# Optimization experiments

Hardware: AMD Instinct MI355X
Metric: run time of the kernel (lower is better)

The kernel has to match this reference:

```python
import jax, jax.numpy as jnp
import numpy as np

N, M, D = 131072, 512, 128  # points, codebook size, feature dim


def setup_inputs() -> dict:
    key = jax.random.key(0)
    k1, k2 = jax.random.split(key)
    X = jax.random.normal(k1, (N, D), dtype=jnp.float32)
    samples = jax.random.normal(k2, (M, D), dtype=jnp.float32)
    return {"X": X, "samples": samples}


def reference(X, samples):
    # Pairwise L2 distance: sum((x - s)^2, axis=-1) ** (1/2), vectorized via
    # for p=2, without materializing an [N, M, D] tensor).
    x2 = jnp.sum(X * X, axis=1, keepdims=True)              # [N, 1]
    s2 = jnp.sum(samples * samples, axis=1)[None, :]        # [1, M]
    d2 = x2 + s2 - 2.0 * (X @ samples.T)                    # [N, M]
    m_dis = jnp.sqrt(jnp.maximum(d2, 0.0))                  # [N, M]
    # soft=True branch: softmax over axis=0 (across points), as in the original.
    return jax.nn.softmax(-m_dis, axis=0)
```

## Files before the change

kernel.cpp:

```cpp
#include <hip/hip_runtime.h>
#include <hip/hip_bf16.h>

#define NPTS 131072
#define MCB  512
#define DIM  128
#define NRB  (NPTS/128)
#define NCBK (MCB/128)
#define NBLK (NRB*NCBK)

typedef __attribute__((ext_vector_type(4))) float  f32x4;
typedef __attribute__((ext_vector_type(8))) __bf16 bf16x8;
typedef unsigned short u16;
typedef unsigned int   u32;

__device__ __forceinline__ u32 swz(u32 p) { return p ^ (((p >> 8) & 7u) << 4); }

__global__ __launch_bounds__(256) void convert_rows(const float* __restrict__ in,
                                                    u16* __restrict__ outb,
                                                    float* __restrict__ sq,
                                                    int nrows) {
  int wv = threadIdx.x >> 6, ln = threadIdx.x & 63;
  int half = ln >> 5, li = ln & 31;
  int npairs = nrows >> 1;
  for (int pr = blockIdx.x * 4 + wv; pr < npairs; pr += gridDim.x * 4) {
    int row = pr * 2 + half;
    const float4 v = *(const float4*)(in + (size_t)row * DIM + li * 4);
    __hip_bfloat16 b0 = __float2bfloat16(v.x);
    __hip_bfloat16 b1 = __float2bfloat16(v.y);
    __hip_bfloat16 b2 = __float2bfloat16(v.z);
    __hip_bfloat16 b3 = __float2bfloat16(v.w);
    ushort4 o;
    o.x = *(const u16*)&b0; o.y = *(const u16*)&b1;
    o.z = *(const u16*)&b2; o.w = *(const u16*)&b3;
    *(ushort4*)(outb + (size_t)row * DIM + li * 4) = o;
    float f0 = __bfloat162float(b0), f1 = __bfloat162float(b1);
    float f2 = __bfloat162float(b2), f3 = __bfloat162float(b3);
    float s = f0 * f0 + f1 * f1 + f2 * f2 + f3 * f3;
    s += __shfl_xor(s, 1); s += __shfl_xor(s, 2); s += __shfl_xor(s, 4);
    s += __shfl_xor(s, 8); s += __shfl_xor(s, 16);
    if (li == 0) sq[row] = s;
  }
}

template <int WRITE>
__global__ __launch_bounds__(256, 2) void gemm_pass(const u16* __restrict__ Xb,
                                                    const u16* __restrict__ Sb,
                                                    const float* __restrict__ x2,
                                                    const float* __restrict__ s2,
                                                    const float* __restrict__ invs,
                                                    float* __restrict__ outp) {
  __shared__ u16 At[128 * DIM];
  __shared__ u16 Bt[128 * DIM];
  __shared__ float lx2[128], ls2[128], lscale[128], colsum[128];

  int t = threadIdx.x, wv = t >> 6, ln = t & 63;
  u32 h = blockIdx.x;
  u32 l = (h & 7u) * (NBLK / 8) + (h >> 3);
  u32 rb = l >> 2, cb = l & 3u;
  u32 n0 = rb * 128, m0 = cb * 128;

  const char* Ag = (const char*)(Xb + (size_t)n0 * DIM);
  const char* Bg = (const char*)(Sb + (size_t)m0 * DIM);
#pragma unroll
  for (int i = 0; i < 8; i++) {
    u32 c = i * 4 + wv;
    u32 lb = c * 1024;
    u32 go = swz(lb + ln * 16);
    __builtin_amdgcn_global_load_lds((const __attribute__((address_space(1))) void*)(Ag + go),
                                     (__attribute__((address_space(3))) void*)((char*)At + lb),
                                     16, 0, 0);
    __builtin_amdgcn_global_load_lds((const __attribute__((address_space(1))) void*)(Bg + go),
                                     (__attribute__((address_space(3))) void*)((char*)Bt + lb),
                                     16, 0, 0);
  }
  if (t < 128) {
    lx2[t] = x2[n0 + t];
    ls2[t] = s2[m0 + t];
    if (WRITE) lscale[t] = invs[m0 + t];
    else       colsum[t] = 0.f;
  }
  __syncthreads();

  int wr = wv >> 1, wc = wv & 1;
  int rbw = wr * 64, cbw = wc * 64;
  int lr = ln & 15, lg = ln >> 4;

  f32x4 acc[4][4];
#pragma unroll
  for (int i = 0; i < 4; i++)
#pragma unroll
    for (int j = 0; j < 4; j++) acc[i][j] = (f32x4){0.f, 0.f, 0.f, 0.f};

#pragma unroll
  for (int kk = 0; kk < 4; kk++) {
    bf16x8 af[4], bfr[4];
#pragma unroll
    for (int i = 0; i < 4; i++)
      af[i] = *(const bf16x8*)((const char*)At +
               swz((u32)((rbw + i * 16 + lr) * 256 + kk * 64 + lg * 16)));
#pragma unroll
    for (int j = 0; j < 4; j++)
      bfr[j] = *(const bf16x8*)((const char*)Bt +
               swz((u32)((cbw + j * 16 + lr) * 256 + kk * 64 + lg * 16)));
#pragma unroll
    for (int i = 0; i < 4; i++)
#pragma unroll
      for (int j = 0; j < 4; j++)
        acc[i][j] = __builtin_amdgcn_mfma_f32_16x16x32_bf16(af[i], bfr[j], acc[i][j], 0, 0, 0);
  }

  float csum[4] = {0.f, 0.f, 0.f, 0.f};
#pragma unroll
  for (int i = 0; i < 4; i++) {
#pragma unroll
    for (int j = 0; j < 4; j++) {
#pragma unroll
      for (int r = 0; r < 4; r++) {
        int nl = rbw + i * 16 + lg * 4 + r;
        int ml = cbw + j * 16 + lr;
        float d2 = lx2[nl] + ls2[ml] - 2.f * acc[i][j][r];
        d2 = fmaxf(d2, 0.f);
        float e = __expf(-__fsqrt_rn(d2));
        if (WRITE) {
          outp[(size_t)(n0 + nl) * MCB + (m0 + ml)] = e * lscale[ml];
        } else {
          csum[j] += e;
        }
      }
    }
  }
  if (!WRITE) {
#pragma unroll
    for (int j = 0; j < 4; j++) {
      float v = csum[j];
      v += __shfl_xor(v, 16);
      v += __shfl_xor(v, 32);
      if (ln < 16) atomicAdd(&colsum[cbw + j * 16 + ln], v);
    }
    __syncthreads();
    if (t < 128) outp[(size_t)rb * MCB + m0 + t] = colsum[t];
  }
}

__global__ __launch_bounds__(256) void reduce_cols(const float* __restrict__ partial,
                                                   float* __restrict__ invs) {
  int m = blockIdx.x, t = threadIdx.x;
  float s = 0.f;
  for (int k = t; k < NRB; k += 256) s += partial[(size_t)k * MCB + m];
  s += __shfl_xor(s, 1);  s += __shfl_xor(s, 2);  s += __shfl_xor(s, 4);
  s += __shfl_xor(s, 8);  s += __shfl_xor(s, 16); s += __shfl_xor(s, 32);
  __shared__ float w4[4];
  if ((t & 63) == 0) w4[t >> 6] = s;
  __syncthreads();
  if (t == 0) invs[m] = 1.0f / (w4[0] + w4[1] + w4[2] + w4[3]);
}

extern "C" void kernel_launch(void* const* d_in, const int* in_sizes, int n_in,
                              void* d_out, int out_size, void* d_ws, size_t ws_size,
                              hipStream_t stream) {
  const float* X = (const float*)d_in[0];
  const float* S = (const float*)d_in[1];
  float* out = (float*)d_out;
  char* ws = (char*)d_ws;

  u16*   Xb      = (u16*)ws;
  u16*   Sb      = (u16*)(ws + 33554432);
  float* x2      = (float*)(ws + 33685504);
  float* s2      = (float*)(ws + 34209792);
  float* invs    = (float*)(ws + 34211840);
  float* partial = (float*)(ws + 34213888);

  convert_rows<<<1024, 256, 0, stream>>>(X, Xb, x2, NPTS);
  convert_rows<<<64, 256, 0, stream>>>(S, Sb, s2, MCB);
  gemm_pass<0><<<NBLK, 256, 0, stream>>>(Xb, Sb, x2, s2, invs, partial);
  reduce_cols<<<MCB, 256, 0, stream>>>(partial, invs);
  gemm_pass<1><<<NBLK, 256, 0, stream>>>(Xb, Sb, x2, s2, invs, out);
}
```

Measured before the change: 372.5 us.

## Load X fragments straight to registers, transpose MFMA for vectorized nontemporal stores

The A tile no longer goes through LDS. Each wave loads its X fragments directly from global memory into registers, which halves LDS use and lets launch bounds rise to 3 blocks per CU. In the write pass the MFMA operands are swapped so each lane holds 4 consecutive columns, so output can be written as float4 nontemporal stores instead of scalar strided stores. The colsum reduction uses per-wave shared slots in place of LDS atomics, and the convert grid is doubled. In exchange there is more register pressure, and the direct global loads are not coalesced as well as the LDS staging was.

```diff
diff --git a/kernel.cpp b/kernel.cpp
--- a/kernel.cpp
+++ b/kernel.cpp
@@ -43,15 +43,15 @@
 }
 
 template <int WRITE>
-__global__ __launch_bounds__(256, 2) void gemm_pass(const u16* __restrict__ Xb,
+__global__ __launch_bounds__(256, 3) void gemm_pass(const u16* __restrict__ Xb,
                                                     const u16* __restrict__ Sb,
                                                     const float* __restrict__ x2,
                                                     const float* __restrict__ s2,
                                                     const float* __restrict__ invs,
                                                     float* __restrict__ outp) {
-  __shared__ u16 At[128 * DIM];
   __shared__ u16 Bt[128 * DIM];
-  __shared__ float lx2[128], ls2[128], lscale[128], colsum[128];
+  __shared__ float lx2[128], ls2[128], lscale[128];
+  __shared__ float colsum2[4][64];
 
   int t = threadIdx.x, wv = t >> 6, ln = t & 63;
   u32 h = blockIdx.x;
@@ -59,32 +59,35 @@
   u32 rb = l >> 2, cb = l & 3u;
   u32 n0 = rb * 128, m0 = cb * 128;
 
-  const char* Ag = (const char*)(Xb + (size_t)n0 * DIM);
   const char* Bg = (const char*)(Sb + (size_t)m0 * DIM);
 #pragma unroll
   for (int i = 0; i < 8; i++) {
-    u32 c = i * 4 + wv;
-    u32 lb = c * 1024;
-    u32 go = swz(lb + ln * 16);
-    __builtin_amdgcn_global_load_lds((const __attribute__((address_space(1))) void*)(Ag + go),
-                                     (__attribute__((address_space(3))) void*)((char*)At + lb),
-                                     16, 0, 0);
+    u32 lb = (u32)(i * 4 + wv) * 1024u;
+    u32 go = swz(lb + (u32)ln * 16u);
     __builtin_amdgcn_global_load_lds((const __attribute__((address_space(1))) void*)(Bg + go),
                                      (__attribute__((address_space(3))) void*)((char*)Bt + lb),
                                      16, 0, 0);
   }
+
+  int wr = wv >> 1, wc = wv & 1;
+  int rbw = wr * 64, cbw = wc * 64;
+  int lr = ln & 15, lg = ln >> 4;
+
+  bf16x8 af[4][4];
+  const u16* Abase = Xb + (size_t)(n0 + rbw) * DIM;
+#pragma unroll
+  for (int i = 0; i < 4; i++)
+#pragma unroll
+    for (int kk = 0; kk < 4; kk++)
+      af[i][kk] = *(const bf16x8*)(Abase + (i * 16 + lr) * DIM + kk * 32 + lg * 8);
+
   if (t < 128) {
     lx2[t] = x2[n0 + t];
     ls2[t] = s2[m0 + t];
     if (WRITE) lscale[t] = invs[m0 + t];
-    else       colsum[t] = 0.f;
   }
   __syncthreads();
 
-  int wr = wv >> 1, wc = wv & 1;
-  int rbw = wr * 64, cbw = wc * 64;
-  int lr = ln & 15, lg = ln >> 4;
-
   f32x4 acc[4][4];
 #pragma unroll
   for (int i = 0; i < 4; i++)
@@ -93,11 +96,7 @@
 
 #pragma unroll
   for (int kk = 0; kk < 4; kk++) {
-    bf16x8 af[4], bfr[4];
-#pragma unroll
-    for (int i = 0; i < 4; i++)
-      af[i] = *(const bf16x8*)((const char*)At +
-               swz((u32)((rbw + i * 16 + lr) * 256 + kk * 64 + lg * 16)));
+    bf16x8 bfr[4];
 #pragma unroll
     for (int j = 0; j < 4; j++)
       bfr[j] = *(const bf16x8*)((const char*)Bt +
@@ -105,40 +104,63 @@
 #pragma unroll
     for (int i = 0; i < 4; i++)
 #pragma unroll
-      for (int j = 0; j < 4; j++)
-        acc[i][j] = __builtin_amdgcn_mfma_f32_16x16x32_bf16(af[i], bfr[j], acc[i][j], 0, 0, 0);
-  }
-
-  float csum[4] = {0.f, 0.f, 0.f, 0.f};
-#pragma unroll
-  for (int i = 0; i < 4; i++) {
-#pragma unroll
-    for (int j = 0; j < 4; j++) {
-#pragma unroll
-      for (int r = 0; r < 4; r++) {
-        int nl = rbw + i * 16 + lg * 4 + r;
-        int ml = cbw + j * 16 + lr;
-        float d2 = lx2[nl] + ls2[ml] - 2.f * acc[i][j][r];
-        d2 = fmaxf(d2, 0.f);
-        float e = __expf(-__fsqrt_rn(d2));
-        if (WRITE) {
-          outp[(size_t)(n0 + nl) * MCB + (m0 + ml)] = e * lscale[ml];
-        } else {
-          csum[j] += e;
+      for (int j = 0; j < 4; j++) {
+        if (WRITE)
+          acc[i][j] = __builtin_amdgcn_mfma_f32_16x16x32_bf16(bfr[j], af[i][kk], acc[i][j], 0, 0, 0);
+        else
+          acc[i][j] = __builtin_amdgcn_mfma_f32_16x16x32_bf16(af[i][kk], bfr[j], acc[i][j], 0, 0, 0);
+      }
+  }
+
+  if (WRITE) {
+#pragma unroll
+    for (int i = 0; i < 4; i++) {
+      int n = rbw + i * 16 + lr;
+      float xx = lx2[n];
+      float* orow = outp + (size_t)(n0 + n) * MCB + m0;
+#pragma unroll
+      for (int j = 0; j < 4; j++) {
+        int mb = cbw + j * 16 + lg * 4;
+        f32x4 v;
+#pragma unroll
+        for (int r = 0; r < 4; r++) {
+          float d2 = xx + ls2[mb + r] - 2.f * acc[i][j][r];
+          d2 = fmaxf(d2, 0.f);
+          float e = __expf(-__fsqrt_rn(d2));
+          v[r] = e * lscale[mb + r];
+        }
+        __builtin_nontemporal_store(v, (f32x4*)(orow + mb));
+      }
+    }
+  } else {
+    float csum[4] = {0.f, 0.f, 0.f, 0.f};
+#pragma unroll
+    for (int i = 0; i < 4; i++) {
+#pragma unroll
+      for (int j = 0; j < 4; j++) {
+        int m = cbw + j * 16 + lr;
+        float ss = ls2[m];
+#pragma unroll
+        for (int r = 0; r < 4; r++) {
+          int n = rbw + i * 16 + lg * 4 + r;
+          float d2 = lx2[n] + ss - 2.f * acc[i][j][r];
+          d2 = fmaxf(d2, 0.f);
+          csum[j] += __expf(-__fsqrt_rn(d2));
         }
       }
     }
-  }
-  if (!WRITE) {
 #pragma unroll
     for (int j = 0; j < 4; j++) {
       float v = csum[j];
       v += __shfl_xor(v, 16);
       v += __shfl_xor(v, 32);
-      if (ln < 16) atomicAdd(&colsum[cbw + j * 16 + ln], v);
+      if (ln < 16) colsum2[wv][j * 16 + ln] = v;
     }
     __syncthreads();
-    if (t < 128) outp[(size_t)rb * MCB + m0 + t] = colsum[t];
+    if (t < 128) {
+      int wcf = t >> 6, lc = t & 63;
+      outp[(size_t)rb * MCB + m0 + t] = colsum2[wcf][lc] + colsum2[wcf + 2][lc];
+    }
   }
 }
 
@@ -170,7 +192,7 @@
   float* invs    = (float*)(ws + 34211840);
   float* partial = (float*)(ws + 34213888);
 
-  convert_rows<<<1024, 256, 0, stream>>>(X, Xb, x2, NPTS);
+  convert_rows<<<2048, 256, 0, stream>>>(X, Xb, x2, NPTS);
   convert_rows<<<64, 256, 0, stream>>>(S, Sb, s2, MCB);
   gemm_pass<0><<<NBLK, 256, 0, stream>>>(Xb, Sb, x2, s2, invs, partial);
   reduce_cols<<<MCB, 256, 0, stream>>>(partial, invs);
```

Result: slower. 398.3 us (+6.9%).
